# Kernel tuning notes

Hardware: AMD Instinct MI355X
Metric: run time of the kernel (lower is better)

The kernel has to match this reference:

```python
import jax, jax.numpy as jnp
import numpy as np

N_NODES = 50000
N_EDGES = 800000
IN_DIM = 128
HID = 64
HEADS = [4, 4, 1]
NUM_CLASSES = 16
NEG_SLOPE = 0.2


def _init_layer(key, in_dim, out_dim, heads):
    k1, k2, k3 = jax.random.split(key, 3)
    W = jax.random.normal(k1, (in_dim, heads * out_dim), jnp.float32) * (1.0 / np.sqrt(in_dim))
    al = jax.random.normal(k2, (heads, out_dim), jnp.float32) * 0.1
    ar = jax.random.normal(k3, (heads, out_dim), jnp.float32) * 0.1
    b = jnp.zeros((heads, out_dim), jnp.float32)
    return W, al, ar, b


def setup_inputs() -> dict:
    key = jax.random.key(0)
    ks = jax.random.split(key, 8)
    inputs = jax.random.normal(ks[0], (N_NODES, IN_DIM), jnp.float32)
    src = jax.random.randint(ks[1], (N_EDGES,), 0, N_NODES, jnp.int32)
    dst = jax.random.randint(ks[2], (N_EDGES,), 0, N_NODES, jnp.int32)
    W0, al0, ar0, b0 = _init_layer(ks[3], IN_DIM, HID, HEADS[0])
    W1, al1, ar1, b1 = _init_layer(ks[4], HID * HEADS[0], HID, HEADS[1])
    W2, al2, ar2, b2 = _init_layer(ks[5], HID * HEADS[1], NUM_CLASSES, HEADS[2])
    return {"inputs": inputs,
            "W0": W0, "al0": al0, "ar0": ar0, "b0": b0,
            "W1": W1, "al1": al1, "ar1": ar1, "b1": b1,
            "W2": W2, "al2": al2, "ar2": ar2, "b2": b2,
            "src": src, "dst": dst}


def gat_layer(h, W, al, ar, b, src, dst):
    # h: [N, F_in]; W: [F_in, H*D]; al/ar/b: [H, D]
    n = h.shape[0]
    H, D = al.shape
    feat = (h @ W).reshape(n, H, D)                 # [N,H,D]
    el = jnp.einsum('nhd,hd->nh', feat, al)          # [N,H]
    er = jnp.einsum('nhd,hd->nh', feat, ar)          # [N,H]
    e = jax.nn.leaky_relu(el[src] + er[dst], NEG_SLOPE)  # [E,H]
    # edge softmax over incoming edges of each dst node
    m = jax.ops.segment_max(e, dst, num_segments=n)
    ee = jnp.exp(e - m[dst])
    s = jax.ops.segment_sum(ee, dst, num_segments=n)
    alpha = ee / s[dst]                              # [E,H]
    msg = feat[src] * alpha[:, :, None]              # [E,H,D]
    out = jax.ops.segment_sum(msg, dst, num_segments=n)  # [N,H,D]
    return out + b


def reference(inputs, W0, al0, ar0, b0, W1, al1, ar1, b1, W2, al2, ar2, b2, src, dst):
    n = inputs.shape[0]
    h = gat_layer(inputs, W0, al0, ar0, b0, src, dst).reshape(n, -1)  # flatten heads
    h = gat_layer(h, W1, al1, ar1, b1, src, dst).reshape(n, -1)
    logits = gat_layer(h, W2, al2, ar2, b2, src, dst).mean(axis=1)    # mean over heads
    return logits
```

## Files before the change

kernel.cpp:

```cpp
#include <hip/hip_runtime.h>
#include <hip/hip_bf16.h>
#include <math.h>


#define NEG_SLOPE 0.2f
#define CAP_E 96

typedef __attribute__((ext_vector_type(8))) _Float16 v8h;
typedef __attribute__((ext_vector_type(2))) _Float16 half2v;
typedef __attribute__((ext_vector_type(4))) float f32x4;


__global__ __launch_bounds__(256) void scatter_edges(const int* __restrict__ src,
                                                     const int* __restrict__ dst,
                                                     int* __restrict__ cnt,
                                                     int* __restrict__ csr, int E) {
    int e = blockIdx.x * 256 + threadIdx.x;
    if (e < E) {
        int d = dst[e];
        int pos = atomicAdd(&cnt[d], 1);
        if (pos < CAP_E) csr[d * CAP_E + pos] = src[e];
    }
}


__device__ __forceinline__ unsigned short f16_bits(float x) {
    _Float16 h = (_Float16)x;
    union { _Float16 h; unsigned short u; } c;
    c.h = h;
    return c.u;
}

__device__ __forceinline__ float f16_to_f32(unsigned short u) {
    union { _Float16 h; unsigned short u; } c;
    c.u = u;
    return (float)c.h;
}

__global__ __launch_bounds__(256) void wcvt2(const float* __restrict__ W0,
                                             unsigned short* __restrict__ t0,
                                             const float* __restrict__ W1,
                                             unsigned short* __restrict__ t1) {
    int idx = blockIdx.x * 256 + threadIdx.x;
    if (idx < 128 * 256) {
        int f = idx >> 8, k = idx & 255;
        t0[k * 128 + f] = f16_bits(W0[idx]);
    } else {
        int j = idx - 128 * 256;
        if (j < 256 * 256) {
            int f = j >> 8, k = j & 255;
            t1[k * 256 + f] = f16_bits(W1[j]);
        }
    }
}


template <bool AF32>
__global__ __launch_bounds__(256) void gemm_mfma(const unsigned short* __restrict__ Af,
                                                 const float* __restrict__ A32,
                                                 const unsigned short* __restrict__ Bt,
                                                 unsigned short* __restrict__ featb,
                                                 float* __restrict__ el,
                                                 float* __restrict__ er,
                                                 const float* __restrict__ al,
                                                 const float* __restrict__ ar,
                                                 int N, int F, int K) {
    __shared__ unsigned short smem[2 * 128 * 40];
    auto As = (unsigned short (*)[40])smem;
    auto Bs = (unsigned short (*)[40])(smem + 128 * 40);
    auto Cs = (unsigned short (*)[136])smem;

    int tid = threadIdx.x;
    int lane = tid & 63, w = tid >> 6;
    int wr = (w >> 1) * 64, wc = (w & 1) * 64;
    int lr = lane & 15, lq = lane >> 4;
    int bid = blockIdx.x + blockIdx.y * 2;
    int g = bid >> 4, b16 = bid & 15;
    int rowb = g * 8 + (b16 & 7);
    int colb = b16 >> 3;
    int m0 = rowb * 128, n0 = colb * 128;
    if (m0 >= N) return;
    f32x4 acc[4][4] = {};

    for (int k0 = 0; k0 < F; k0 += 32) {
        __syncthreads();
#pragma unroll
        for (int i = 0; i < 2; ++i) {
            int slot = i * 256 + tid;
            int r = slot >> 2, cc = slot & 3;
            int gr = m0 + r;
            uint4 v = make_uint4(0u, 0u, 0u, 0u);
            if (AF32) {
                if (gr < N) {
                    const float* p = &A32[(size_t)gr * F + k0 + cc * 8];
                    float4 f0 = *(const float4*)p;
                    float4 f1 = *(const float4*)(p + 4);
                    v.x = (unsigned)f16_bits(f0.x) | ((unsigned)f16_bits(f0.y) << 16);
                    v.y = (unsigned)f16_bits(f0.z) | ((unsigned)f16_bits(f0.w) << 16);
                    v.z = (unsigned)f16_bits(f1.x) | ((unsigned)f16_bits(f1.y) << 16);
                    v.w = (unsigned)f16_bits(f1.z) | ((unsigned)f16_bits(f1.w) << 16);
                }
            } else {
                if (gr < N) v = *(const uint4*)&Af[(size_t)gr * F + k0 + cc * 8];
            }
            *(uint4*)&As[r][cc * 8] = v;
        }
#pragma unroll
        for (int i = 0; i < 2; ++i) {
            int slot = i * 256 + tid;
            int r = slot >> 2, cc = slot & 3;
            uint4 bv = *(const uint4*)&Bt[(size_t)(n0 + r) * F + k0 + cc * 8];
            *(uint4*)&Bs[r][cc * 8] = bv;
        }
        __syncthreads();

        v8h af[4], bf[4];
#pragma unroll
        for (int mt = 0; mt < 4; ++mt)
            af[mt] = *(const v8h*)&As[wr + mt * 16 + lr][lq * 8];
#pragma unroll
        for (int nt = 0; nt < 4; ++nt)
            bf[nt] = *(const v8h*)&Bs[wc + nt * 16 + lr][lq * 8];
#pragma unroll
        for (int mt = 0; mt < 4; ++mt)
#pragma unroll
            for (int nt = 0; nt < 4; ++nt)
                acc[mt][nt] = __builtin_amdgcn_mfma_f32_16x16x32_f16(af[mt], bf[nt], acc[mt][nt], 0, 0, 0);
    }

    int h = (n0 + wc) >> 6;
    float alw[4], arw[4];
#pragma unroll
    for (int nt = 0; nt < 4; ++nt) {
        int d = nt * 16 + lr;
        alw[nt] = al[h * 64 + d];
        arw[nt] = ar[h * 64 + d];
    }
#pragma unroll
    for (int mt = 0; mt < 4; ++mt) {
#pragma unroll
        for (int r = 0; r < 4; ++r) {
            float se = 0.f, sr = 0.f;
#pragma unroll
            for (int nt = 0; nt < 4; ++nt) {
                float v = acc[mt][nt][r];
                se += v * alw[nt];
                sr += v * arw[nt];
            }
#pragma unroll
            for (int o = 8; o >= 1; o >>= 1) {
                se += __shfl_xor(se, o);
                sr += __shfl_xor(sr, o);
            }
            int row = m0 + wr + mt * 16 + lq * 4 + r;
            if (lr == 0 && row < N) {
                el[(size_t)row * 4 + h] = se;
                er[(size_t)row * 4 + h] = sr;
            }
        }
    }

#pragma unroll
    for (int half = 0; half < 2; ++half) {
        __syncthreads();
#pragma unroll
        for (int mtl = 0; mtl < 2; ++mtl) {
            int mt = half * 2 + mtl;
            int cr = (wr >> 1) + mtl * 16 + lq * 4;
#pragma unroll
            for (int nt = 0; nt < 4; ++nt) {
                int col = wc + nt * 16 + lr;
#pragma unroll
                for (int r = 0; r < 4; ++r)
                    Cs[cr + r][col] = f16_bits(acc[mt][nt][r]);
            }
        }
        __syncthreads();
        int cr = tid >> 2, seg = (tid & 3) * 32;
        int grow = m0 + (cr & 31) + ((cr >> 5) << 6) + half * 32;
        if (grow < N) {
            uint4* dst4 = (uint4*)&featb[(size_t)grow * K + n0 + seg];
            const uint4* src4 = (const uint4*)&Cs[cr][seg];
            dst4[0] = src4[0];
            dst4[1] = src4[1];
            dst4[2] = src4[2];
            dst4[3] = src4[3];
        }
    }
}


__global__ __launch_bounds__(256) void gemm2_mfma(const unsigned short* __restrict__ Af,
                                                  const float* __restrict__ W,
                                                  const float* __restrict__ al2,
                                                  const float* __restrict__ ar2,
                                                  float* __restrict__ el,
                                                  float* __restrict__ er,
                                                  unsigned short* __restrict__ featb,
                                                  int N) {
    int tid = threadIdx.x;
    int wv = tid >> 6, lane = tid & 63;
    int lr = lane & 15, lq = lane >> 4;
    int m0 = blockIdx.x * 256 + wv * 64;
    if (m0 >= N) return;

    v8h bh[8], bl[8];
#pragma unroll
    for (int kk = 0; kk < 8; ++kk) {
#pragma unroll
        for (int j = 0; j < 8; ++j) {
            float wval = W[(kk * 32 + lq * 8 + j) * 16 + lr];
            _Float16 hi = (_Float16)wval;
            _Float16 lo = (_Float16)(wval - (float)hi);
            bh[kk][j] = hi;
            bl[kk][j] = lo;
        }
    }

    f32x4 acc[4] = {};
#pragma unroll
    for (int kk = 0; kk < 8; ++kk) {
        v8h af[4];
#pragma unroll
        for (int mt = 0; mt < 4; ++mt) {
            int row = m0 + mt * 16 + lr;
            v8h a = {};
            if (row < N) a = *(const v8h*)&Af[(size_t)row * 256 + kk * 32 + lq * 8];
            af[mt] = a;
        }
#pragma unroll
        for (int mt = 0; mt < 4; ++mt) {
            acc[mt] = __builtin_amdgcn_mfma_f32_16x16x32_f16(af[mt], bh[kk], acc[mt], 0, 0, 0);
            acc[mt] = __builtin_amdgcn_mfma_f32_16x16x32_f16(af[mt], bl[kk], acc[mt], 0, 0, 0);
        }
    }

    float alv = al2[lr], arv = ar2[lr];
#pragma unroll
    for (int mt = 0; mt < 4; ++mt) {
#pragma unroll
        for (int r = 0; r < 4; ++r) {
            int row = m0 + mt * 16 + lq * 4 + r;
            float v = acc[mt][r];
            float pe = v * alv, pr = v * arv;
            pe += __shfl_xor(pe, 1); pr += __shfl_xor(pr, 1);
            pe += __shfl_xor(pe, 2); pr += __shfl_xor(pr, 2);
            pe += __shfl_xor(pe, 4); pr += __shfl_xor(pr, 4);
            pe += __shfl_xor(pe, 8); pr += __shfl_xor(pr, 8);
            if (row < N) {
                if (lr == 0) { el[row] = pe; er[row] = pr; }
                featb[(size_t)row * 16 + lr] = f16_bits(v);
            }
        }
    }
}


template <int U>
__global__ __launch_bounds__(256) void agg4_kernel(const unsigned short* __restrict__ featb,
                                                   const float* __restrict__ el,
                                                   const float* __restrict__ er,
                                                   const float* __restrict__ bias,
                                                   const int* __restrict__ cnt,
                                                   const int* __restrict__ csr,
                                                   unsigned short* __restrict__ outh, int N) {
    constexpr int CAP = 32;
    __shared__ float s_alpha[8][4][33];
    __shared__ int s_src[8][CAP];
    int hw = threadIdx.x >> 5;
    int cl = threadIdx.x & 31;
    int n = blockIdx.x * 8 + hw;
    if (n >= N) return;
    int begin = n * CAP_E;
    int deg = cnt[n];
    deg = deg < CAP_E ? deg : CAP_E;
    float4 ern = *(const float4*)&er[(size_t)n * 4];

    const v8h* frow8 = (const v8h*)featb;
    int h2 = cl >> 3;
    int dcap = deg < CAP ? deg : CAP;

    float s0 = 0.f, s1 = 0.f, s2 = 0.f, s3 = 0.f;
    v8h g0[U];
    float a0[U];
    int nbe = 0;

    if (deg <= CAP) {
        bool act = cl < deg;
        float x0 = 0.f, x1 = 0.f, x2 = 0.f, x3 = 0.f;
        if (act) {
            int s = csr[begin + cl];
            float4 e = *(const float4*)&el[(size_t)s * 4];
            float e0 = e.x + ern.x, e1 = e.y + ern.y, e2 = e.z + ern.z, e3 = e.w + ern.w;
            e0 = e0 > 0.f ? e0 : NEG_SLOPE * e0;
            e1 = e1 > 0.f ? e1 : NEG_SLOPE * e1;
            e2 = e2 > 0.f ? e2 : NEG_SLOPE * e2;
            e3 = e3 > 0.f ? e3 : NEG_SLOPE * e3;
            x0 = __expf(e0); x1 = __expf(e1);
            x2 = __expf(e2); x3 = __expf(e3);
            s_src[hw][cl] = s;
            s_alpha[hw][0][cl] = x0;
            s_alpha[hw][1][cl] = x1;
            s_alpha[hw][2][cl] = x2;
            s_alpha[hw][3][cl] = x3;
        }
        if (dcap > 0) {
            nbe = dcap < U ? dcap : U;
#pragma unroll
            for (int u = 0; u < U; ++u) {
                if (u < nbe) {
                    int s = s_src[hw][u];
                    g0[u] = frow8[(size_t)s * 32 + cl];
                    a0[u] = s_alpha[hw][h2][u];
                }
            }
        }
        s0 = x0; s1 = x1; s2 = x2; s3 = x3;
#pragma unroll
        for (int o = 16; o >= 1; o >>= 1) {
            s0 += __shfl_xor(s0, o); s1 += __shfl_xor(s1, o);
            s2 += __shfl_xor(s2, o); s3 += __shfl_xor(s3, o);
        }
    } else {
        for (int i = cl; i < deg; i += 32) {
            int s = csr[begin + i];
            float4 e = *(const float4*)&el[(size_t)s * 4];
            float e0 = e.x + ern.x, e1 = e.y + ern.y, e2 = e.z + ern.z, e3 = e.w + ern.w;
            e0 = e0 > 0.f ? e0 : NEG_SLOPE * e0;
            e1 = e1 > 0.f ? e1 : NEG_SLOPE * e1;
            e2 = e2 > 0.f ? e2 : NEG_SLOPE * e2;
            e3 = e3 > 0.f ? e3 : NEG_SLOPE * e3;
            float x0 = __expf(e0), x1 = __expf(e1), x2 = __expf(e2), x3 = __expf(e3);
            if (i < CAP) {
                s_src[hw][i] = s;
                s_alpha[hw][0][i] = x0; s_alpha[hw][1][i] = x1;
                s_alpha[hw][2][i] = x2; s_alpha[hw][3][i] = x3;
            }
            s0 += x0; s1 += x1; s2 += x2; s3 += x3;
        }
#pragma unroll
        for (int o = 16; o >= 1; o >>= 1) {
            s0 += __shfl_xor(s0, o); s1 += __shfl_xor(s1, o);
            s2 += __shfl_xor(s2, o); s3 += __shfl_xor(s3, o);
        }
    }

    float inv0 = deg > 0 ? 1.f / s0 : 0.f;
    float inv1 = deg > 0 ? 1.f / s1 : 0.f;
    float inv2 = deg > 0 ? 1.f / s2 : 0.f;
    float inv3 = deg > 0 ? 1.f / s3 : 0.f;
    float inv = h2 == 0 ? inv0 : (h2 == 1 ? inv1 : (h2 == 2 ? inv2 : inv3));

    float c[8] = {};
    int j = 0;
    if (nbe > 0) {
#pragma unroll
        for (int u = 0; u < U; ++u) {
            if (u < nbe) {
#pragma unroll
                for (int k = 0; k < 8; ++k) c[k] += a0[u] * (float)g0[u][k];
            }
        }
        j = nbe;
    }
    for (; j + U <= dcap; j += U) {
        int s[U];
        v8h gv[U];
        float a[U];
#pragma unroll
        for (int u = 0; u < U; ++u) s[u] = s_src[hw][j + u];
#pragma unroll
        for (int u = 0; u < U; ++u) gv[u] = frow8[(size_t)s[u] * 32 + cl];
#pragma unroll
        for (int u = 0; u < U; ++u) a[u] = s_alpha[hw][h2][j + u];
#pragma unroll
        for (int u = 0; u < U; ++u) {
#pragma unroll
            for (int k = 0; k < 8; ++k) c[k] += a[u] * (float)gv[u][k];
        }
    }
    for (; j < dcap; ++j) {
        int s = s_src[hw][j];
        v8h gv = frow8[(size_t)s * 32 + cl];
        float a = s_alpha[hw][h2][j];
#pragma unroll
        for (int k = 0; k < 8; ++k) c[k] += a * (float)gv[k];
    }
    if (deg > CAP) {
        float ernh = h2 == 0 ? ern.x : (h2 == 1 ? ern.y : (h2 == 2 ? ern.z : ern.w));
        for (int i = CAP; i < deg; ++i) {
            int s = csr[begin + i];
            float eh = el[(size_t)s * 4 + h2] + ernh;
            eh = eh > 0.f ? eh : NEG_SLOPE * eh;
            float a = __expf(eh);
            v8h gv = frow8[(size_t)s * 32 + cl];
#pragma unroll
            for (int k = 0; k < 8; ++k) c[k] += a * (float)gv[k];
        }
    }
    float4 ba = *(const float4*)&bias[8 * cl];
    float4 bb = *(const float4*)&bias[8 * cl + 4];
    float o0 = c[0] * inv + ba.x;
    float o1 = c[1] * inv + ba.y;
    float o2 = c[2] * inv + ba.z;
    float o3 = c[3] * inv + ba.w;
    float o4 = c[4] * inv + bb.x;
    float o5 = c[5] * inv + bb.y;
    float o6 = c[6] * inv + bb.z;
    float o7 = c[7] * inv + bb.w;
    uint4 pk;
    pk.x = (unsigned int)f16_bits(o0) | ((unsigned int)f16_bits(o1) << 16);
    pk.y = (unsigned int)f16_bits(o2) | ((unsigned int)f16_bits(o3) << 16);
    pk.z = (unsigned int)f16_bits(o4) | ((unsigned int)f16_bits(o5) << 16);
    pk.w = (unsigned int)f16_bits(o6) | ((unsigned int)f16_bits(o7) << 16);
    ((uint4*)outh)[(size_t)n * 32 + cl] = pk;
}


template <int CAP>
__global__ __launch_bounds__(256) void agg16_kernel(const unsigned short* __restrict__ featb,
                                                    const float* __restrict__ el,
                                                    const float* __restrict__ er,
                                                    const float* __restrict__ bias,
                                                    const int* __restrict__ cnt,
                                                    const int* __restrict__ csr,
                                                    float* __restrict__ out, int N) {
    __shared__ float s_alpha[4][CAP];
    __shared__ int s_src[4][CAP];
    int w = threadIdx.x >> 6;
    int lane = threadIdx.x & 63;
    int n = blockIdx.x * 4 + w;
    if (n >= N) return;
    int begin = n * CAP_E;
    int deg = cnt[n];
    deg = deg < CAP_E ? deg : CAP_E;
    float ern = er[n];

    float ssum = 0.f;
    if (deg <= 64) {
        bool act = lane < deg;
        float x = 0.f;
        if (act) {
            int s = csr[begin + lane];
            float e = el[s] + ern;
            e = e > 0.f ? e : NEG_SLOPE * e;
            x = __expf(e);
            s_src[w][lane] = s;
            s_alpha[w][lane] = x;
        }
        ssum = x;
#pragma unroll
        for (int o = 32; o >= 1; o >>= 1) ssum += __shfl_xor(ssum, o);
    } else {
        for (int i = lane; i < deg; i += 64) {
            int s = csr[begin + i];
            float e = el[s] + ern;
            e = e > 0.f ? e : NEG_SLOPE * e;
            float x = __expf(e);
            if (i < CAP) { s_src[w][i] = s; s_alpha[w][i] = x; }
            ssum += x;
        }
#pragma unroll
        for (int o = 32; o >= 1; o >>= 1) ssum += __shfl_xor(ssum, o);
    }
    float inv = deg > 0 ? 1.f / ssum : 0.f;

    int slot = lane >> 3, p = lane & 7;
    int dcap = deg < CAP ? deg : CAP;
    const half2v* frow = (const half2v*)featb;
    float ax = 0.f, ay = 0.f;
    for (int j = slot; j < dcap; j += 8) {
        int s = s_src[w][j];
        float a = s_alpha[w][j];
        half2v f = frow[(size_t)s * 8 + p];
        ax += a * (float)f[0];
        ay += a * (float)f[1];
    }
    for (int i = CAP + slot; i < deg; i += 8) {
        int s = csr[begin + i];
        float e = el[s] + ern;
        e = e > 0.f ? e : NEG_SLOPE * e;
        float x = __expf(e);
        half2v f = frow[(size_t)s * 8 + p];
        ax += x * (float)f[0];
        ay += x * (float)f[1];
    }
#pragma unroll
    for (int o = 8; o < 64; o <<= 1) {
        ax += __shfl_xor(ax, o);
        ay += __shfl_xor(ay, o);
    }
    if (lane < 8) {
        float2 o2 = make_float2(ax * inv + bias[2 * p], ay * inv + bias[2 * p + 1]);
        *(float2*)&out[(size_t)n * 16 + 2 * p] = o2;
    }
}


extern "C" void kernel_launch(void* const* d_in, const int* in_sizes, int n_in,
                              void* d_out, int out_size, void* d_ws, size_t ws_size,
                              hipStream_t stream) {
    const float* inputs = (const float*)d_in[0];
    const float* W0 = (const float*)d_in[1];
    const float* al0 = (const float*)d_in[2];
    const float* ar0 = (const float*)d_in[3];
    const float* b0 = (const float*)d_in[4];
    const float* W1 = (const float*)d_in[5];
    const float* al1 = (const float*)d_in[6];
    const float* ar1 = (const float*)d_in[7];
    const float* b1 = (const float*)d_in[8];
    const float* W2 = (const float*)d_in[9];
    const float* al2 = (const float*)d_in[10];
    const float* ar2 = (const float*)d_in[11];
    const float* b2 = (const float*)d_in[12];
    const int* src = (const int*)d_in[13];
    const int* dst = (const int*)d_in[14];

    const int IN_DIM = 128;
    const int N = in_sizes[0] / IN_DIM;
    const int E = in_sizes[13];
    float* out = (float*)d_out;

    char* base = (char*)d_ws;
    size_t o = 0;
    auto carve = [&](size_t bytes) -> void* {
        void* p = base + o;
        o += (bytes + 255) & ~(size_t)255;
        return p;
    };
    int* cnt = (int*)carve((size_t)N * sizeof(int));
    int* csr = (int*)carve((size_t)N * CAP_E * sizeof(int));
    float* el = (float*)carve((size_t)N * 4 * sizeof(float));
    float* er = (float*)carve((size_t)N * 4 * sizeof(float));
    unsigned short* featb = (unsigned short*)carve((size_t)N * 256 * sizeof(unsigned short));
    unsigned short* hbf = (unsigned short*)carve((size_t)N * 256 * sizeof(unsigned short));
    unsigned short* wt0 = (unsigned short*)carve((size_t)128 * 256 * sizeof(unsigned short));
    unsigned short* wt1 = (unsigned short*)carve((size_t)256 * 256 * sizeof(unsigned short));

    hipMemsetAsync(cnt, 0, (size_t)N * sizeof(int), stream);
    int egrid = (E + 255) / 256;
    scatter_edges<<<egrid, 256, 0, stream>>>(src, dst, cnt, csr, E);

    wcvt2<<<(128 * 256 + 256 * 256 + 255) / 256, 256, 0, stream>>>(W0, wt0, W1, wt1);

    int rowsP = (((N + 127) / 128) + 7) & ~7;
    {
        dim3 grid(2, rowsP);
        gemm_mfma<true><<<grid, 256, 0, stream>>>(nullptr, inputs, wt0, featb, el, er, al0, ar0, N, 128, 256);
        agg4_kernel<4><<<(N + 7) / 8, 256, 0, stream>>>(featb, el, er, b0, cnt, csr, hbf, N);
    }
    {
        dim3 grid(2, rowsP);
        gemm_mfma<false><<<grid, 256, 0, stream>>>(hbf, nullptr, wt1, featb, el, er, al1, ar1, N, 256, 256);
        agg4_kernel<4><<<(N + 7) / 8, 256, 0, stream>>>(featb, el, er, b1, cnt, csr, hbf, N);
    }
    {
        gemm2_mfma<<<(N + 255) / 256, 256, 0, stream>>>(hbf, W2, al2, ar2, el, er, featb, N);
        agg16_kernel<64><<<(N + 3) / 4, 256, 0, stream>>>(featb, el, er, b2, cnt, csr, out, N);
    }
}
```

Before: 353.3 us.

## Fuse edge scatter with layer-0 GEMM and fold count reset into weight prep

```diff
diff --git a/kernel.cpp b/kernel.cpp
--- a/kernel.cpp
+++ b/kernel.cpp
@@ -5,23 +5,11 @@
 
 #define NEG_SLOPE 0.2f
 #define CAP_E 96
+#define SCAT_B 256
 
 typedef __attribute__((ext_vector_type(8))) _Float16 v8h;
 typedef __attribute__((ext_vector_type(2))) _Float16 half2v;
 typedef __attribute__((ext_vector_type(4))) float f32x4;
-
-
-__global__ __launch_bounds__(256) void scatter_edges(const int* __restrict__ src,
-                                                     const int* __restrict__ dst,
-                                                     int* __restrict__ cnt,
-                                                     int* __restrict__ csr, int E) {
-    int e = blockIdx.x * 256 + threadIdx.x;
-    if (e < E) {
-        int d = dst[e];
-        int pos = atomicAdd(&cnt[d], 1);
-        if (pos < CAP_E) csr[d * CAP_E + pos] = src[e];
-    }
-}
 
 
 __device__ __forceinline__ unsigned short f16_bits(float x) {
@@ -37,34 +25,38 @@
     return (float)c.h;
 }
 
-__global__ __launch_bounds__(256) void wcvt2(const float* __restrict__ W0,
-                                             unsigned short* __restrict__ t0,
-                                             const float* __restrict__ W1,
-                                             unsigned short* __restrict__ t1) {
+
+__global__ __launch_bounds__(256) void prep(const float* __restrict__ W0,
+                                            unsigned short* __restrict__ t0,
+                                            const float* __restrict__ W1,
+                                            unsigned short* __restrict__ t1,
+                                            int* __restrict__ cnt, int N) {
     int idx = blockIdx.x * 256 + threadIdx.x;
-    if (idx < 128 * 256) {
-        int f = idx >> 8, k = idx & 255;
-        t0[k * 128 + f] = f16_bits(W0[idx]);
-    } else {
-        int j = idx - 128 * 256;
-        if (j < 256 * 256) {
-            int f = j >> 8, k = j & 255;
-            t1[k * 256 + f] = f16_bits(W1[j]);
-        }
+    if (idx < N) cnt[idx] = 0;
+    int j0 = idx - N;
+    if (j0 >= 0 && j0 < 128 * 256) {
+        int f = j0 >> 8, k = j0 & 255;
+        t0[k * 128 + f] = f16_bits(W0[j0]);
+    }
+    int j1 = idx - N - 128 * 256;
+    if (j1 >= 0 && j1 < 256 * 256) {
+        int f = j1 >> 8, k = j1 & 255;
+        t1[k * 256 + f] = f16_bits(W1[j1]);
     }
 }
 
 
 template <bool AF32>
-__global__ __launch_bounds__(256) void gemm_mfma(const unsigned short* __restrict__ Af,
-                                                 const float* __restrict__ A32,
-                                                 const unsigned short* __restrict__ Bt,
-                                                 unsigned short* __restrict__ featb,
-                                                 float* __restrict__ el,
-                                                 float* __restrict__ er,
-                                                 const float* __restrict__ al,
-                                                 const float* __restrict__ ar,
-                                                 int N, int F, int K) {
+__device__ __forceinline__ void gemm_body(int bid,
+                                          const unsigned short* __restrict__ Af,
+                                          const float* __restrict__ A32,
+                                          const unsigned short* __restrict__ Bt,
+                                          unsigned short* __restrict__ featb,
+                                          float* __restrict__ el,
+                                          float* __restrict__ er,
+                                          const float* __restrict__ al,
+                                          const float* __restrict__ ar,
+                                          int N, int F, int K) {
     __shared__ unsigned short smem[2 * 128 * 40];
     auto As = (unsigned short (*)[40])smem;
     auto Bs = (unsigned short (*)[40])(smem + 128 * 40);
@@ -74,7 +66,6 @@
     int lane = tid & 63, w = tid >> 6;
     int wr = (w >> 1) * 64, wc = (w & 1) * 64;
     int lr = lane & 15, lq = lane >> 4;
-    int bid = blockIdx.x + blockIdx.y * 2;
     int g = bid >> 4, b16 = bid & 15;
     int rowb = g * 8 + (b16 & 7);
     int colb = b16 >> 3;
@@ -187,6 +178,44 @@
             dst4[3] = src4[3];
         }
     }
+}
+
+
+__global__ __launch_bounds__(256) void scatter_gemm0(const int* __restrict__ src,
+                                                     const int* __restrict__ dst,
+                                                     int* __restrict__ cnt,
+                                                     int* __restrict__ csr, int E,
+                                                     const float* __restrict__ A32,
+                                                     const unsigned short* __restrict__ Bt,
+                                                     unsigned short* __restrict__ featb,
+                                                     float* __restrict__ el,
+                                                     float* __restrict__ er,
+                                                     const float* __restrict__ al,
+                                                     const float* __restrict__ ar,
+                                                     int N) {
+    if (blockIdx.x < SCAT_B) {
+        int stride = SCAT_B * 256;
+        for (int e = blockIdx.x * 256 + threadIdx.x; e < E; e += stride) {
+            int d = dst[e];
+            int pos = atomicAdd(&cnt[d], 1);
+            if (pos < CAP_E) csr[d * CAP_E + pos] = src[e];
+        }
+    } else {
+        gemm_body<true>(blockIdx.x - SCAT_B, nullptr, A32, Bt, featb, el, er, al, ar, N, 128, 256);
+    }
+}
+
+
+__global__ __launch_bounds__(256) void gemm_l1(const unsigned short* __restrict__ Af,
+                                               const unsigned short* __restrict__ Bt,
+                                               unsigned short* __restrict__ featb,
+                                               float* __restrict__ el,
+                                               float* __restrict__ er,
+                                               const float* __restrict__ al,
+                                               const float* __restrict__ ar,
+                                               int N) {
+    int bid = blockIdx.x + blockIdx.y * 2;
+    gemm_body<false>(bid, Af, nullptr, Bt, featb, el, er, al, ar, N, 256, 256);
 }
 
 
@@ -537,21 +566,17 @@
     unsigned short* wt0 = (unsigned short*)carve((size_t)128 * 256 * sizeof(unsigned short));
     unsigned short* wt1 = (unsigned short*)carve((size_t)256 * 256 * sizeof(unsigned short));
 
-    hipMemsetAsync(cnt, 0, (size_t)N * sizeof(int), stream);
-    int egrid = (E + 255) / 256;
-    scatter_edges<<<egrid, 256, 0, stream>>>(src, dst, cnt, csr, E);
-
-    wcvt2<<<(128 * 256 + 256 * 256 + 255) / 256, 256, 0, stream>>>(W0, wt0, W1, wt1);
+    int prepTotal = N + 128 * 256 + 256 * 256;
+    prep<<<(prepTotal + 255) / 256, 256, 0, stream>>>(W0, wt0, W1, wt1, cnt, N);
 
     int rowsP = (((N + 127) / 128) + 7) & ~7;
+    scatter_gemm0<<<SCAT_B + 2 * rowsP, 256, 0, stream>>>(src, dst, cnt, csr, E,
+                                                          inputs, wt0, featb, el, er, al0, ar0, N);
+    agg4_kernel<4><<<(N + 7) / 8, 256, 0, stream>>>(featb, el, er, b0, cnt, csr, hbf, N);
+
     {
         dim3 grid(2, rowsP);
-        gemm_mfma<true><<<grid, 256, 0, stream>>>(nullptr, inputs, wt0, featb, el, er, al0, ar0, N, 128, 256);
-        agg4_kernel<4><<<(N + 7) / 8, 256, 0, stream>>>(featb, el, er, b0, cnt, csr, hbf, N);
-    }
-    {
-        dim3 grid(2, rowsP);
-        gemm_mfma<false><<<grid, 256, 0, stream>>>(hbf, nullptr, wt1, featb, el, er, al1, ar1, N, 256, 256);
+        gemm_l1<<<grid, 256, 0, stream>>>(hbf, wt1, featb, el, er, al1, ar1, N);
         agg4_kernel<4><<<(N + 7) / 8, 256, 0, stream>>>(featb, el, er, b1, cnt, csr, hbf, N);
     }
     {
```

New measurement: 332.9 us, median of 2. 5.8% less time.
